# Kernel tuning notes

Measured on AMD Instinct MI355X. Metric: run time of the kernel, lower is better.

Reference implementation:

```python
import jax, jax.numpy as jnp
import numpy as np

# Dimensions inferred from the module (few-shot reweighted YOLOv2 region loss)
B, C, NA, NCPA = 64, 20, 5, 1          # batch, base classes, anchors, classes-per-anchor
H, W = 19, 19                           # feature map (608 input / stride 32)
T = 50                                  # cfg.max_boxes
THRESH = 0.6
COORD_SCALE = 1.0
CLASS_SCALE = 1.0
NB = B * C                              # per-class 'image' rows, as in the torch code
A4 = NA * H * W
EPS = 1e-12
BCE_EPS = 1e-7
ANCHORS = [[1.3221, 1.73145], [3.19275, 4.00944], [5.05587, 8.09892], [9.47112, 4.84053], [11.2364, 10.0071]]


def iou_xywh(x1, y1, w1, h1, x2, y2, w2, h2):
    # center-size IoU, matches darknet bbox_iou(x1y1x2y2=False)
    l = jnp.maximum(x1 - w1 * 0.5, x2 - w2 * 0.5)
    r = jnp.minimum(x1 + w1 * 0.5, x2 + w2 * 0.5)
    t = jnp.maximum(y1 - h1 * 0.5, y2 - h2 * 0.5)
    b = jnp.minimum(y1 + h1 * 0.5, y2 + h2 * 0.5)
    inter = jnp.clip(r - l, 0.0) * jnp.clip(b - t, 0.0)
    union = w1 * h1 + w2 * h2 - inter
    return inter / jnp.maximum(union, EPS)


def setup_inputs() -> dict:
    key = jax.random.key(0)
    k1, k2, k3, k4 = jax.random.split(key, 4)
    output = jax.random.normal(k1, (NB, NA * (5 + NCPA), H, W), jnp.float32) * 0.5
    # target rows: [cls, x, y, w, h] * T, coords in (0,1); x kept > 0 so all boxes are 'valid'
    cls_ids = jax.random.randint(k2, (B, C, T), 0, C).astype(jnp.float32)
    xy = jax.random.uniform(k3, (B, C, T, 2), minval=0.05, maxval=0.95)
    wh = jax.random.uniform(k4, (B, C, T, 2), minval=0.05, maxval=0.5)
    target = jnp.concatenate([cls_ids[..., None], xy, wh], axis=-1).reshape(B, C, T * 5)
    anchors = jnp.asarray(ANCHORS, jnp.float32)
    return {"output": output, "target": target, "anchors": anchors}


def _forward(output, target, anchors):
    target = jax.lax.stop_gradient(target)
    anchors = jax.lax.stop_gradient(anchors)
    out5 = output.reshape(NB, NA, 5 + NCPA, H, W)
    x = jax.nn.sigmoid(out5[:, :, 0])
    y = jax.nn.sigmoid(out5[:, :, 1])
    w = out5[:, :, 2]
    h = out5[:, :, 3]
    conf = jax.nn.sigmoid(out5[:, :, 4])
    # class logits regrouped to original batch: (B*NA*H*W, C)
    cls = out5[:, :, 5:5 + NCPA].reshape(NB, NA, H, W)
    cls_logits = cls.reshape(B, C, NA * H * W).transpose(0, 2, 1).reshape(-1, C)
    # decode pred boxes (detached, mirroring torch's use of .data)
    grid_x = jnp.arange(W, dtype=jnp.float32)[None, None, None, :]
    grid_y = jnp.arange(H, dtype=jnp.float32)[None, None, :, None]
    aw = anchors[:, 0][None, :, None, None]
    ah = anchors[:, 1][None, :, None, None]
    px = jax.lax.stop_gradient(x) + grid_x
    py = jax.lax.stop_gradient(y) + grid_y
    pw = jnp.exp(jax.lax.stop_gradient(w)) * aw
    ph = jnp.exp(jax.lax.stop_gradient(h)) * ah
    # ground-truth boxes per row
    tgt = target.reshape(NB, T, 5)
    cls_t = tgt[:, :, 0]
    gx = tgt[:, :, 1] * W
    gy = tgt[:, :, 2] * H
    gw = tgt[:, :, 3] * W
    gh = tgt[:, :, 4] * H
    # 'break on first zero x' semantics
    valid = jnp.cumprod((tgt[:, :, 1] != 0).astype(jnp.int32), axis=1) > 0
    # stage 1: zero conf_mask where any gt IoU > thresh (scan over T to avoid (NB,T,A4) blowup)
    pxf = px.reshape(NB, A4); pyf = py.reshape(NB, A4)
    pwf = pw.reshape(NB, A4); phf = ph.reshape(NB, A4)

    def iou_step(ci, xs):
        gxt, gyt, gwt, ght, vt = xs
        iou = iou_xywh(pxf, pyf, pwf, phf, gxt[:, None], gyt[:, None], gwt[:, None], ght[:, None])
        return jnp.maximum(ci, jnp.where(vt[:, None], iou, 0.0)), None

    cur_ious, _ = jax.lax.scan(iou_step, jnp.zeros((NB, A4), jnp.float32), (gx.T, gy.T, gw.T, gh.T, valid.T))
    conf_mask0 = jnp.where(cur_ious.reshape(NB, NA, H, W) > THRESH, 0.0, 1.0)
    # best anchor per gt by wh-only IoU
    inter = jnp.minimum(gw[..., None], anchors[:, 0]) * jnp.minimum(gh[..., None], anchors[:, 1])
    union = gw[..., None] * gh[..., None] + anchors[:, 0] * anchors[:, 1] - inter
    best_n = jnp.argmax(inter / jnp.maximum(union, EPS), axis=-1).astype(jnp.int32)  # (NB,T)
    gi = gx.astype(jnp.int32)
    gj = gy.astype(jnp.int32)
    # stage 2: ordered scatter of targets (later boxes overwrite earlier, as in the torch loops)
    binds = jnp.arange(NB)
    z = jnp.zeros((NB, NA, H, W), jnp.float32)
    # seen < 12800 branch: tx=ty=0.5, tw=th=0, coord_mask=1
    carry0 = (jnp.ones_like(z), z, conf_mask0, jnp.full_like(z, 0.5), jnp.full_like(z, 0.5), z, z, z, z)

    def tgt_step(carry, xs):
        cm, clm, cfm, tx, ty, tw, th, tconf, tcls = carry
        gxt, gyt, gwt, ght, bn, git, gjt, vt, ct = xs
        idx = (binds, bn, gjt, git)

        def upd(arr, val):
            return arr.at[idx].set(jnp.where(vt, val, arr[idx]))

        aw_b = anchors[bn, 0]
        ah_b = anchors[bn, 1]
        iou = iou_xywh(gxt, gyt, gwt, ght, px[idx], py[idx], pw[idx], ph[idx])
        cm = upd(cm, 1.0)
        clm = upd(clm, 1.0)
        cfm = upd(cfm, 1.0)
        tx = upd(tx, gxt - git.astype(jnp.float32))
        ty = upd(ty, gyt - gjt.astype(jnp.float32))
        tw = upd(tw, jnp.log(jnp.maximum(gwt, EPS) / aw_b))
        th = upd(th, jnp.log(jnp.maximum(ght, EPS) / ah_b))
        tconf = upd(tconf, iou)
        tcls = upd(tcls, ct)
        return (cm, clm, cfm, tx, ty, tw, th, tconf, tcls), None

    xs = (gx.T, gy.T, gw.T, gh.T, best_n.T, gi.T, gj.T, valid.T, cls_t.T)
    (coord_mask, cls_mask, conf_mask, tx, ty, tw, th, tconf, tcls), _ = jax.lax.scan(tgt_step, carry0, xs)
    # regroup per-class rows back to original batch (neg_ratio='full' -> counts[i] == C)
    cm_grp = cls_mask.reshape(B, C, NA, H, W).sum(axis=1)
    tcls_grp = tcls.reshape(B, C, NA, H, W).sum(axis=1)
    sel = (cm_grp == 1.0).reshape(-1)           # exclude colliding cells
    labels = tcls_grp.reshape(-1).astype(jnp.int32)

    def bce_mean(p, t):
        p = jnp.clip(p, BCE_EPS, 1.0 - BCE_EPS)
        return jnp.mean(-(t * jnp.log(p) + (1.0 - t) * jnp.log(1.0 - p)))

    loss_x = COORD_SCALE * bce_mean(x * coord_mask, tx * coord_mask)
    loss_y = COORD_SCALE * bce_mean(y * coord_mask, ty * coord_mask)
    loss_w = COORD_SCALE * 0.5 * jnp.mean((w * coord_mask - tw * coord_mask) ** 2)
    loss_h = COORD_SCALE * 0.5 * jnp.mean((h * coord_mask - th * coord_mask) ** 2)
    loss_conf = 0.5 * jnp.mean((conf * conf_mask - tconf * conf_mask) ** 2)
    logp = jax.nn.log_softmax(cls_logits, axis=-1)
    nll = -jnp.take_along_axis(logp, labels[:, None], axis=1)[:, 0]
    nsel = jnp.maximum(jnp.sum(sel.astype(jnp.float32)), 1.0)
    loss_cls = CLASS_SCALE * jnp.sum(jnp.where(sel, nll, 0.0)) / nsel
    return loss_x + loss_y + loss_w + loss_h + loss_conf + loss_cls


def reference(output, target, anchors):
    return _forward(output, target, anchors)
```

## Files before the change

kernel.cpp:

```cpp
#include <hip/hip_runtime.h>
#include <math.h>

constexpr int cB   = 64;
constexpr int cC   = 20;
constexpr int cNA  = 5;
constexpr int cH   = 19;
constexpr int cW   = 19;
constexpr int cT   = 50;
constexpr int cNB  = cB * cC;
constexpr int cHW  = cH * cW;
constexpr int cA4  = cNA * cHW;
constexpr int cCH  = cNA * 6;
constexpr long cNTOT = (long)cNB * cA4;
constexpr int cCLS_BLOCKS = cB * cNA;

__device__ __constant__ float cAW[cNA]   = {1.3221f, 3.19275f, 5.05587f, 9.47112f, 11.2364f};
__device__ __constant__ float cAH[cNA]   = {1.73145f, 4.00944f, 8.09892f, 4.84053f, 10.0071f};
__device__ __constant__ float cAREA[cNA] = {2.28930345f, 12.80114796f, 40.94706183f, 45.84455262f, 112.44377644f};
__device__ __constant__ float cLNAW[cNA] = {0.27920469f, 1.16088088f, 1.62060702f, 2.24822684f, 2.41915174f};
__device__ __constant__ float cLNAH[cNA] = {0.54896100f, 1.38865236f, 2.09173157f, 1.57701337f, 2.30329495f};

constexpr int ACC_BANKS = 64;
constexpr size_t OFF_CNT = 2560;
constexpr size_t OFF_ROW = 4096;
constexpr size_t ZERO_BYTES = OFF_ROW + (size_t)cB * cA4 * 4;

__device__ __forceinline__ float fexp(float x) {
    return __builtin_amdgcn_exp2f(x * 1.4426950408889634f);
}
__device__ __forceinline__ float flog(float x) {
    return __builtin_amdgcn_logf(x) * 0.6931471805599453f;
}
__device__ __forceinline__ float frcp(float x) { return __builtin_amdgcn_rcpf(x); }
__device__ __forceinline__ float fsigmoid(float x) { return frcp(1.0f + fexp(-x)); }

typedef _Float16 h2 __attribute__((ext_vector_type(2)));
union HU { unsigned u; h2 h; };
__device__ __forceinline__ unsigned splat2(float v) {
    HU x; _Float16 f = (_Float16)v; x.h[0] = f; x.h[1] = f; return x.u;
}
constexpr float cS = 1.2649110640673518f;

__launch_bounds__(256)
__global__ void k_main(const float* __restrict__ outp, const float* __restrict__ target,
                       int* __restrict__ rowenc, double* __restrict__ acc) {
    __shared__ int s_win[cA4];
    __shared__ int s_tc[cT];
    __shared__ __align__(16) unsigned s_box[cT][8];
    __shared__ __align__(16) float4 s_gt[cT];
    __shared__ double s_red[3][4];
    const int tid  = threadIdx.x;
    const int nb   = blockIdx.x >> 1;
    const int half = blockIdx.x & 1;
    const int base = (half << 10) + tid;
    const int b_   = nb / cC;
    const int c_   = nb - b_ * cC;
    const float* obase = outp + (size_t)nb * (cCH * cHW);

    for (int k = tid; k < cA4; k += 256) s_win[k] = -1;
    __syncthreads();

    if (tid < 64) {
        const int t = tid;
        float xr = 1.f, yr = 0.f, wr = 0.f, hr = 0.f;
        if (t < cT) {
            const float* tg = target + (size_t)nb * (cT * 5) + t * 5;
            xr = tg[1]; yr = tg[2]; wr = tg[3]; hr = tg[4];
        }
        unsigned long long nz = __ballot(xr != 0.0f);
        if (t < cT) {
            unsigned long long below = (2ull << t) - 1ull;
            bool valid = ((~nz) & below) == 0ull;
            float gx = xr * (float)cW, gy = yr * (float)cH;
            float gw = wr * (float)cW, gh = hr * (float)cH;
            s_gt[t] = make_float4(gx, gy, gw, gh);
            if (valid) {
                s_box[t][0] = splat2(cS * (gx - 0.5f * gw));
                s_box[t][1] = splat2(cS * (gx + 0.5f * gw));
                s_box[t][2] = splat2(cS * (gy - 0.5f * gh));
                s_box[t][3] = splat2(cS * (gy + 0.5f * gh));
                s_box[t][4] = splat2(-0.6f * (gw * gh));
                float garea = gw * gh;
                float best = -1.0f; int bn = 0;
                for (int n = 0; n < cNA; ++n) {
                    float inter = fminf(gw, cAW[n]) * fminf(gh, cAH[n]);
                    float uni   = garea + cAREA[n] - inter;
                    float r = inter / fmaxf(uni, 1e-12f);
                    if (r > best) { best = r; bn = n; }
                }
                int cell = bn * cHW + (int)gy * cW + (int)gx;
                s_tc[t] = cell;
                atomicMax(&s_win[cell], t);
            } else {
                s_box[t][0] = splat2(1e4f);  s_box[t][1] = splat2(-1e4f);
                s_box[t][2] = splat2(1e4f);  s_box[t][3] = splat2(-1e4f);
                s_box[t][4] = splat2(0.0f);
                s_tc[t] = -1;
            }
        }
    }
    __syncthreads();
    if (half == 0 && tid < cT) {
        int cell = s_tc[tid];
        if (cell >= 0 && s_win[cell] == tid)
            atomicAdd(&rowenc[b_ * cA4 + cell], (1 << 10) | (c_ * cT + tid));
    }

    h2 pl2[2], pr2[2], pt2[2], pb2[2], ov2[2], pa06h[2];
    float conf[4], tcf[4];
    unsigned wbits = 0;
    float bce = 0.0f, sq = 0.0f;
    const h2 z2 = { (_Float16)0.0f, (_Float16)0.0f };

    #pragma unroll
    for (int u = 0; u < 4; ++u) {
        int cell = base + (u << 8);
        bool a_  = cell < cA4;
        int cc   = a_ ? cell : (cA4 - 1);
        int na   = cc / cHW;
        int rem  = cc - na * cHW;
        int j    = rem / cW;
        int i    = rem - j * cW;
        const float* ob = obase + (size_t)(na * 6) * cHW + rem;
        float xl = ob[0], yl = ob[cHW], wl = ob[2*cHW], hl = ob[3*cHW], cl = ob[4*cHW];
        float aw = cAW[na], ah = cAH[na];
        float x  = fsigmoid(xl), y = fsigmoid(yl), cf = fsigmoid(cl);
        float px = x + (float)i, py = y + (float)j;
        float pw = fexp(wl) * aw, ph = fexp(hl) * ah;
        float l0 = px - 0.5f*pw, r0 = px + 0.5f*pw;
        float t0 = py - 0.5f*ph, b0 = py + 0.5f*ph;
        float pa = pw * ph;
        int p = u >> 1, s = u & 1;
        pl2[p][s] = (_Float16)(cS * l0);  pr2[p][s] = (_Float16)(cS * r0);
        pt2[p][s] = (_Float16)(cS * t0);  pb2[p][s] = (_Float16)(cS * b0);
        pa06h[p][s] = (_Float16)(0.6f * pa);
        ov2[p][s] = (_Float16)0.0f;
        conf[u] = cf; tcf[u] = 0.0f;

        float tx = 0.5f, ty = 0.5f, tw = 0.0f, th = 0.0f;
        int wt = s_win[cc];
        bool wfl = (wt >= 0) && a_;
        if (wfl) {
            wbits |= (1u << u);
            float4 g = s_gt[wt];
            float gx = g.x, gy = g.y, gw = g.z, gh = g.w;
            tx = gx - (float)i; ty = gy - (float)j;
            tw = flog(fmaxf(gw, 1e-12f)) - cLNAW[na];
            th = flog(fmaxf(gh, 1e-12f)) - cLNAH[na];
            float iw = fminf(r0, gx + 0.5f*gw) - fmaxf(l0, gx - 0.5f*gw);
            float ih = fminf(b0, gy + 0.5f*gh) - fmaxf(t0, gy - 0.5f*gh);
            iw = fmaxf(iw, 0.0f); ih = fmaxf(ih, 0.0f);
            float inter = iw * ih;
            float uni   = gw*gh + pa - inter;
            tcf[u] = inter * frcp(fmaxf(uni, 1e-12f));
        }
        if (a_) {
            float pc = fminf(fmaxf(x, 1e-7f), 1.0f - 1e-7f);
            bce += -(tx * flog(pc) + (1.0f - tx) * flog(1.0f - pc));
            pc = fminf(fmaxf(y, 1e-7f), 1.0f - 1e-7f);
            bce += -(ty * flog(pc) + (1.0f - ty) * flog(1.0f - pc));
            float dw = wl - tw, dh = hl - th;
            sq += dw*dw + dh*dh;
        }
    }

    #pragma unroll 10
    for (int t = 0; t < cT; ++t) {
        uint4 bx = *(const uint4*)&s_box[t][0];
        unsigned gv = s_box[t][4];
        HU a, b, c, d, e;
        a.u = bx.x; b.u = bx.y; c.u = bx.z; d.u = bx.w; e.u = gv;
        #pragma unroll
        for (int p = 0; p < 2; ++p) {
            h2 iw = __builtin_elementwise_min(pr2[p], b.h) - __builtin_elementwise_max(pl2[p], a.h);
            h2 ih = __builtin_elementwise_min(pb2[p], d.h) - __builtin_elementwise_max(pt2[p], c.h);
            iw = __builtin_elementwise_max(iw, z2);
            ih = __builtin_elementwise_max(ih, z2);
            ov2[p] = __builtin_elementwise_max(ov2[p], iw * ih + e.h);
        }
    }

    float sc = 0.0f;
    #pragma unroll
    for (int u = 0; u < 4; ++u) {
        int cell = base + (u << 8);
        if (cell >= cA4) continue;
        int p = u >> 1, s = u & 1;
        bool wfl  = (wbits >> u) & 1;
        bool over = ov2[p][s] > pa06h[p][s];
        float cm  = wfl ? 1.0f : (over ? 0.0f : 1.0f);
        float d   = (conf[u] - tcf[u]) * cm;
        sc += d * d;
    }

    double v0 = (double)bce, v1 = (double)sq, v2 = (double)sc;
    for (int off = 32; off > 0; off >>= 1) {
        v0 += __shfl_down(v0, off);
        v1 += __shfl_down(v1, off);
        v2 += __shfl_down(v2, off);
    }
    int lane = tid & 63, wid = tid >> 6;
    if (lane == 0) { s_red[0][wid] = v0; s_red[1][wid] = v1; s_red[2][wid] = v2; }
    __syncthreads();
    if (tid == 0) {
        double a0 = s_red[0][0] + s_red[0][1] + s_red[0][2] + s_red[0][3];
        double a1 = s_red[1][0] + s_red[1][1] + s_red[1][2] + s_red[1][3];
        double a2 = s_red[2][0] + s_red[2][1] + s_red[2][2] + s_red[2][3];
        int bank = blockIdx.x & (ACC_BANKS - 1);
        atomicAdd(&acc[0*ACC_BANKS + bank], a0);
        atomicAdd(&acc[1*ACC_BANKS + bank], a1);
        atomicAdd(&acc[2*ACC_BANKS + bank], a2);
    }
}

__launch_bounds__(384)
__global__ void k_cls(const float* __restrict__ outp, const float* __restrict__ target,
                      const int* __restrict__ rowenc, double* __restrict__ acc,
                      int* __restrict__ cnt, float* __restrict__ out) {
    __shared__ double s_red[2][6];
    __shared__ int s_last;
    const int tid = threadIdx.x;
    const int b   = blockIdx.x / cNA;
    const int na  = blockIdx.x - b * cNA;
    double nll = 0.0, ns = 0.0;
    if (tid < cHW) {
        const int rem = tid;
        const float* ob = outp + ((size_t)(b * cC) * cCH + na * 6 + 5) * cHW + rem;
        float l[cC]; float m = -1e30f;
        #pragma unroll
        for (int c = 0; c < cC; ++c) {
            l[c] = ob[(size_t)c * (cCH * cHW)];
            m = fmaxf(m, l[c]);
        }
        float s = 0.0f;
        #pragma unroll
        for (int c = 0; c < cC; ++c) s += fexp(l[c] - m);
        float lse = m + flog(s);
        int row = b * cA4 + na * cHW + rem;
        int v = rowenc[row];
        if ((v >> 10) == 1) {
            int payload = v & 1023;
            int selc = payload / cT;
            int selt = payload - selc * cT;
            int label = (int)target[((size_t)(b * cC + selc) * cT + selt) * 5];
            nll = (double)(lse - l[label]);
            ns  = 1.0;
        }
    }
    for (int off = 32; off > 0; off >>= 1) {
        nll += __shfl_down(nll, off);
        ns  += __shfl_down(ns, off);
    }
    int lane = tid & 63, wid = tid >> 6;
    if (lane == 0) { s_red[0][wid] = nll; s_red[1][wid] = ns; }
    __syncthreads();
    if (tid == 0) {
        double a0 = 0.0, a1 = 0.0;
        #pragma unroll
        for (int w = 0; w < 6; ++w) { a0 += s_red[0][w]; a1 += s_red[1][w]; }
        int bank = blockIdx.x & (ACC_BANKS - 1);
        atomicAdd(&acc[3*ACC_BANKS + bank], a0);
        atomicAdd(&acc[4*ACC_BANKS + bank], a1);
        __threadfence();
        s_last = (atomicAdd(cnt, 1) == cCLS_BLOCKS - 1);
    }
    __syncthreads();
    if (s_last && tid < 64) {
        __threadfence();
        double s[5];
        #pragma unroll
        for (int j = 0; j < 5; ++j) {
            double v = atomicAdd(&acc[j * ACC_BANKS + tid], 0.0);
            for (int off = 32; off > 0; off >>= 1) v += __shfl_down(v, off);
            s[j] = v;
        }
        if (tid == 0) {
            double Ninv = 1.0 / (double)cNTOT;
            double loss = s[0] * Ninv
                        + 0.5 * s[1] * Ninv
                        + 0.5 * s[2] * Ninv
                        + s[3] / fmax(s[4], 1.0);
            out[0] = (float)loss;
        }
    }
}

extern "C" void kernel_launch(void* const* d_in, const int* in_sizes, int n_in,
                              void* d_out, int out_size, void* d_ws, size_t ws_size,
                              hipStream_t stream) {
    const float* output = (const float*)d_in[0];
    const float* target = (const float*)d_in[1];
    char* ws = (char*)d_ws;
    double* acc    = (double*)ws;
    int*    cnt    = (int*)(ws + OFF_CNT);
    int*    rowenc = (int*)(ws + OFF_ROW);

    hipMemsetAsync(ws, 0, ZERO_BYTES, stream);

    k_main<<<cNB * 2, 256, 0, stream>>>(output, target, rowenc, acc);
    k_cls<<<cCLS_BLOCKS, 384, 0, stream>>>(output, target, rowenc, acc, cnt, (float*)d_out);
}
```

Measured before the change: 128.9 us.

## Drop memset and atomics; recompute class winners in cls kernel, use per-block partials

Removes the hipMemsetAsync launch and the global atomic rowenc table. The class kernel now recomputes per-class target winners for its (batch, anchor) slice in shared memory, and both kernels write per-block partial sums that the last block reduces. The cnt reset moves into k_main. The class-logit loads and softmax now run only for selected cells. This removes one launch and the atomic contention, at the cost of redundant target parsing in k_cls.

Result: slower. 134.4 us (+4.3%).

```diff
diff --git a/kernel.cpp b/kernel.cpp
--- a/kernel.cpp
+++ b/kernel.cpp
@@ -12,7 +12,8 @@
 constexpr int cA4  = cNA * cHW;
 constexpr int cCH  = cNA * 6;
 constexpr long cNTOT = (long)cNB * cA4;
-constexpr int cCLS_BLOCKS = cB * cNA;
+constexpr int cMAIN_BLOCKS = cNB * 2;
+constexpr int cCLS_BLOCKS  = cB * cNA;
 
 __device__ __constant__ float cAW[cNA]   = {1.3221f, 3.19275f, 5.05587f, 9.47112f, 11.2364f};
 __device__ __constant__ float cAH[cNA]   = {1.73145f, 4.00944f, 8.09892f, 4.84053f, 10.0071f};
@@ -20,10 +21,9 @@
 __device__ __constant__ float cLNAW[cNA] = {0.27920469f, 1.16088088f, 1.62060702f, 2.24822684f, 2.41915174f};
 __device__ __constant__ float cLNAH[cNA] = {0.54896100f, 1.38865236f, 2.09173157f, 1.57701337f, 2.30329495f};
 
-constexpr int ACC_BANKS = 64;
-constexpr size_t OFF_CNT = 2560;
-constexpr size_t OFF_ROW = 4096;
-constexpr size_t ZERO_BYTES = OFF_ROW + (size_t)cB * cA4 * 4;
+constexpr size_t OFF_P1  = 0;
+constexpr size_t OFF_CNT = (size_t)cMAIN_BLOCKS * 3 * 8;
+constexpr size_t OFF_P2  = OFF_CNT + 64;
 
 __device__ __forceinline__ float fexp(float x) {
     return __builtin_amdgcn_exp2f(x * 1.4426950408889634f);
@@ -43,9 +43,8 @@
 
 __launch_bounds__(256)
 __global__ void k_main(const float* __restrict__ outp, const float* __restrict__ target,
-                       int* __restrict__ rowenc, double* __restrict__ acc) {
+                       double* __restrict__ part1, int* __restrict__ cnt) {
     __shared__ int s_win[cA4];
-    __shared__ int s_tc[cT];
     __shared__ __align__(16) unsigned s_box[cT][8];
     __shared__ __align__(16) float4 s_gt[cT];
     __shared__ double s_red[3][4];
@@ -53,9 +52,9 @@
     const int nb   = blockIdx.x >> 1;
     const int half = blockIdx.x & 1;
     const int base = (half << 10) + tid;
-    const int b_   = nb / cC;
-    const int c_   = nb - b_ * cC;
     const float* obase = outp + (size_t)nb * (cCH * cHW);
+
+    if (blockIdx.x == 0 && tid == 0) *cnt = 0;
 
     for (int k = tid; k < cA4; k += 256) s_win[k] = -1;
     __syncthreads();
@@ -89,22 +88,15 @@
                     if (r > best) { best = r; bn = n; }
                 }
                 int cell = bn * cHW + (int)gy * cW + (int)gx;
-                s_tc[t] = cell;
                 atomicMax(&s_win[cell], t);
             } else {
                 s_box[t][0] = splat2(1e4f);  s_box[t][1] = splat2(-1e4f);
                 s_box[t][2] = splat2(1e4f);  s_box[t][3] = splat2(-1e4f);
                 s_box[t][4] = splat2(0.0f);
-                s_tc[t] = -1;
             }
         }
     }
     __syncthreads();
-    if (half == 0 && tid < cT) {
-        int cell = s_tc[tid];
-        if (cell >= 0 && s_win[cell] == tid)
-            atomicAdd(&rowenc[b_ * cA4 + cell], (1 << 10) | (c_ * cT + tid));
-    }
 
     h2 pl2[2], pr2[2], pt2[2], pb2[2], ov2[2], pa06h[2];
     float conf[4], tcf[4];
@@ -203,45 +195,76 @@
     if (lane == 0) { s_red[0][wid] = v0; s_red[1][wid] = v1; s_red[2][wid] = v2; }
     __syncthreads();
     if (tid == 0) {
-        double a0 = s_red[0][0] + s_red[0][1] + s_red[0][2] + s_red[0][3];
-        double a1 = s_red[1][0] + s_red[1][1] + s_red[1][2] + s_red[1][3];
-        double a2 = s_red[2][0] + s_red[2][1] + s_red[2][2] + s_red[2][3];
-        int bank = blockIdx.x & (ACC_BANKS - 1);
-        atomicAdd(&acc[0*ACC_BANKS + bank], a0);
-        atomicAdd(&acc[1*ACC_BANKS + bank], a1);
-        atomicAdd(&acc[2*ACC_BANKS + bank], a2);
+        part1[(size_t)blockIdx.x * 3 + 0] = s_red[0][0] + s_red[0][1] + s_red[0][2] + s_red[0][3];
+        part1[(size_t)blockIdx.x * 3 + 1] = s_red[1][0] + s_red[1][1] + s_red[1][2] + s_red[1][3];
+        part1[(size_t)blockIdx.x * 3 + 2] = s_red[2][0] + s_red[2][1] + s_red[2][2] + s_red[2][3];
     }
 }
 
 __launch_bounds__(384)
 __global__ void k_cls(const float* __restrict__ outp, const float* __restrict__ target,
-                      const int* __restrict__ rowenc, double* __restrict__ acc,
+                      const double* __restrict__ part1, double* __restrict__ part2,
                       int* __restrict__ cnt, float* __restrict__ out) {
+    __shared__ int s_win[cC * cHW];
     __shared__ double s_red[2][6];
+    __shared__ double s_fin[5][6];
     __shared__ int s_last;
-    const int tid = threadIdx.x;
-    const int b   = blockIdx.x / cNA;
-    const int na  = blockIdx.x - b * cNA;
+    const int tid  = threadIdx.x;
+    const int wave = tid >> 6;
+    const int lane = tid & 63;
+    const int b    = blockIdx.x / cNA;
+    const int na   = blockIdx.x - b * cNA;
+
+    for (int k = tid; k < cC * cHW; k += 384) s_win[k] = -1;
+    __syncthreads();
+
+    for (int c = wave; c < cC; c += 6) {
+        const float* tg = target + (size_t)(b * cC + c) * (cT * 5);
+        float xr = 1.f, yr = 0.f, wr = 0.f, hr = 0.f;
+        if (lane < cT) { xr = tg[lane*5+1]; yr = tg[lane*5+2]; wr = tg[lane*5+3]; hr = tg[lane*5+4]; }
+        unsigned long long nz = __ballot(xr != 0.0f);
+        if (lane < cT) {
+            unsigned long long below = (2ull << lane) - 1ull;
+            bool valid = ((~nz) & below) == 0ull;
+            if (valid) {
+                float gx = xr * (float)cW, gy = yr * (float)cH;
+                float gw = wr * (float)cW, gh = hr * (float)cH;
+                float garea = gw * gh;
+                float best = -1.0f; int bn = 0;
+                for (int n = 0; n < cNA; ++n) {
+                    float inter = fminf(gw, cAW[n]) * fminf(gh, cAH[n]);
+                    float uni   = garea + cAREA[n] - inter;
+                    float r = inter / fmaxf(uni, 1e-12f);
+                    if (r > best) { best = r; bn = n; }
+                }
+                if (bn == na)
+                    atomicMax(&s_win[c * cHW + (int)gy * cW + (int)gx], lane);
+            }
+        }
+    }
+    __syncthreads();
+
     double nll = 0.0, ns = 0.0;
     if (tid < cHW) {
         const int rem = tid;
-        const float* ob = outp + ((size_t)(b * cC) * cCH + na * 6 + 5) * cHW + rem;
-        float l[cC]; float m = -1e30f;
+        int cntc = 0, selc = -1, selt = -1;
         #pragma unroll
         for (int c = 0; c < cC; ++c) {
-            l[c] = ob[(size_t)c * (cCH * cHW)];
-            m = fmaxf(m, l[c]);
-        }
-        float s = 0.0f;
-        #pragma unroll
-        for (int c = 0; c < cC; ++c) s += fexp(l[c] - m);
-        float lse = m + flog(s);
-        int row = b * cA4 + na * cHW + rem;
-        int v = rowenc[row];
-        if ((v >> 10) == 1) {
-            int payload = v & 1023;
-            int selc = payload / cT;
-            int selt = payload - selc * cT;
+            int wv = s_win[c * cHW + rem];
+            if (wv >= 0) { cntc++; selc = c; selt = wv; }
+        }
+        if (cntc == 1) {
+            const float* ob = outp + ((size_t)(b * cC) * cCH + na * 6 + 5) * cHW + rem;
+            float l[cC]; float m = -1e30f;
+            #pragma unroll
+            for (int c = 0; c < cC; ++c) {
+                l[c] = ob[(size_t)c * (cCH * cHW)];
+                m = fmaxf(m, l[c]);
+            }
+            float s = 0.0f;
+            #pragma unroll
+            for (int c = 0; c < cC; ++c) s += fexp(l[c] - m);
+            float lse = m + flog(s);
             int label = (int)target[((size_t)(b * cC + selc) * cT + selt) * 5];
             nll = (double)(lse - l[label]);
             ns  = 1.0;
@@ -251,30 +274,48 @@
         nll += __shfl_down(nll, off);
         ns  += __shfl_down(ns, off);
     }
-    int lane = tid & 63, wid = tid >> 6;
-    if (lane == 0) { s_red[0][wid] = nll; s_red[1][wid] = ns; }
+    if (lane == 0) { s_red[0][wave] = nll; s_red[1][wave] = ns; }
     __syncthreads();
     if (tid == 0) {
         double a0 = 0.0, a1 = 0.0;
         #pragma unroll
         for (int w = 0; w < 6; ++w) { a0 += s_red[0][w]; a1 += s_red[1][w]; }
-        int bank = blockIdx.x & (ACC_BANKS - 1);
-        atomicAdd(&acc[3*ACC_BANKS + bank], a0);
-        atomicAdd(&acc[4*ACC_BANKS + bank], a1);
+        part2[(size_t)blockIdx.x * 2 + 0] = a0;
+        part2[(size_t)blockIdx.x * 2 + 1] = a1;
         __threadfence();
         s_last = (atomicAdd(cnt, 1) == cCLS_BLOCKS - 1);
     }
     __syncthreads();
-    if (s_last && tid < 64) {
+
+    if (s_last) {
         __threadfence();
-        double s[5];
+        double v[5] = {0.0, 0.0, 0.0, 0.0, 0.0};
+        for (int k = tid; k < cMAIN_BLOCKS; k += 384) {
+            v[0] += part1[(size_t)k * 3 + 0];
+            v[1] += part1[(size_t)k * 3 + 1];
+            v[2] += part1[(size_t)k * 3 + 2];
+        }
+        for (int k = tid; k < cCLS_BLOCKS; k += 384) {
+            v[3] += atomicAdd(&part2[(size_t)k * 2 + 0], 0.0);
+            v[4] += atomicAdd(&part2[(size_t)k * 2 + 1], 0.0);
+        }
         #pragma unroll
-        for (int j = 0; j < 5; ++j) {
-            double v = atomicAdd(&acc[j * ACC_BANKS + tid], 0.0);
-            for (int off = 32; off > 0; off >>= 1) v += __shfl_down(v, off);
-            s[j] = v;
-        }
+        for (int j = 0; j < 5; ++j)
+            for (int off = 32; off > 0; off >>= 1) v[j] += __shfl_down(v[j], off);
+        if (lane == 0) {
+            #pragma unroll
+            for (int j = 0; j < 5; ++j) s_fin[j][wave] = v[j];
+        }
+        __syncthreads();
         if (tid == 0) {
+            double s[5];
+            #pragma unroll
+            for (int j = 0; j < 5; ++j) {
+                double a = 0.0;
+                #pragma unroll
+                for (int w = 0; w < 6; ++w) a += s_fin[j][w];
+                s[j] = a;
+            }
             double Ninv = 1.0 / (double)cNTOT;
             double loss = s[0] * Ninv
                         + 0.5 * s[1] * Ninv
@@ -291,12 +332,10 @@
     const float* output = (const float*)d_in[0];
     const float* target = (const float*)d_in[1];
     char* ws = (char*)d_ws;
-    double* acc    = (double*)ws;
-    int*    cnt    = (int*)(ws + OFF_CNT);
-    int*    rowenc = (int*)(ws + OFF_ROW);
-
-    hipMemsetAsync(ws, 0, ZERO_BYTES, stream);
-
-    k_main<<<cNB * 2, 256, 0, stream>>>(output, target, rowenc, acc);
-    k_cls<<<cCLS_BLOCKS, 384, 0, stream>>>(output, target, rowenc, acc, cnt, (float*)d_out);
-}
+    double* part1 = (double*)(ws + OFF_P1);
+    int*    cnt   = (int*)   (ws + OFF_CNT);
+    double* part2 = (double*)(ws + OFF_P2);
+
+    k_main<<<cMAIN_BLOCKS, 256, 0, stream>>>(output, target, part1, cnt);
+    k_cls<<<cCLS_BLOCKS, 384, 0, stream>>>(output, target, part1, part2, cnt, (float*)d_out);
+}
```

## Merge k_main half-blocks into one 512-thread block; split k_cls blocks in two

Applied to the files above, without the earlier changes.

k_main now runs one 512-thread block per class-image row instead of two 256-thread halves. The target preprocessing, IoU setup and shared-memory init that each half repeated now run once per row. k_cls is split into twice as many 192-thread blocks, each covering half the grid cells of an anchor, so the gather-heavy class loss uses more, smaller blocks. The trade-off is fewer, larger main blocks, which puts more register pressure on each CU and may lower its occupancy.

New measurement: 133.8 us. +3.8%, slower.

```diff
diff --git a/kernel.cpp b/kernel.cpp
--- a/kernel.cpp
+++ b/kernel.cpp
@@ -12,7 +12,7 @@
 constexpr int cA4  = cNA * cHW;
 constexpr int cCH  = cNA * 6;
 constexpr long cNTOT = (long)cNB * cA4;
-constexpr int cCLS_BLOCKS = cB * cNA;
+constexpr int cCLS_BLOCKS = cB * cNA * 2;
 
 __device__ __constant__ float cAW[cNA]   = {1.3221f, 3.19275f, 5.05587f, 9.47112f, 11.2364f};
 __device__ __constant__ float cAH[cNA]   = {1.73145f, 4.00944f, 8.09892f, 4.84053f, 10.0071f};
@@ -41,23 +41,21 @@
 }
 constexpr float cS = 1.2649110640673518f;
 
-__launch_bounds__(256)
+__launch_bounds__(512, 8)
 __global__ void k_main(const float* __restrict__ outp, const float* __restrict__ target,
                        int* __restrict__ rowenc, double* __restrict__ acc) {
     __shared__ int s_win[cA4];
     __shared__ int s_tc[cT];
     __shared__ __align__(16) unsigned s_box[cT][8];
     __shared__ __align__(16) float4 s_gt[cT];
-    __shared__ double s_red[3][4];
-    const int tid  = threadIdx.x;
-    const int nb   = blockIdx.x >> 1;
-    const int half = blockIdx.x & 1;
-    const int base = (half << 10) + tid;
-    const int b_   = nb / cC;
-    const int c_   = nb - b_ * cC;
+    __shared__ double s_red[3][8];
+    const int tid = threadIdx.x;
+    const int nb  = blockIdx.x;
+    const int b_  = nb / cC;
+    const int c_  = nb - b_ * cC;
     const float* obase = outp + (size_t)nb * (cCH * cHW);
 
-    for (int k = tid; k < cA4; k += 256) s_win[k] = -1;
+    for (int k = tid; k < cA4; k += 512) s_win[k] = -1;
     __syncthreads();
 
     if (tid < 64) {
@@ -100,7 +98,7 @@
         }
     }
     __syncthreads();
-    if (half == 0 && tid < cT) {
+    if (tid < cT) {
         int cell = s_tc[tid];
         if (cell >= 0 && s_win[cell] == tid)
             atomicAdd(&rowenc[b_ * cA4 + cell], (1 << 10) | (c_ * cT + tid));
@@ -114,7 +112,7 @@
 
     #pragma unroll
     for (int u = 0; u < 4; ++u) {
-        int cell = base + (u << 8);
+        int cell = tid + (u << 9);
         bool a_  = cell < cA4;
         int cc   = a_ ? cell : (cA4 - 1);
         int na   = cc / cHW;
@@ -183,7 +181,7 @@
     float sc = 0.0f;
     #pragma unroll
     for (int u = 0; u < 4; ++u) {
-        int cell = base + (u << 8);
+        int cell = tid + (u << 9);
         if (cell >= cA4) continue;
         int p = u >> 1, s = u & 1;
         bool wfl  = (wbits >> u) & 1;
@@ -203,28 +201,31 @@
     if (lane == 0) { s_red[0][wid] = v0; s_red[1][wid] = v1; s_red[2][wid] = v2; }
     __syncthreads();
     if (tid == 0) {
-        double a0 = s_red[0][0] + s_red[0][1] + s_red[0][2] + s_red[0][3];
-        double a1 = s_red[1][0] + s_red[1][1] + s_red[1][2] + s_red[1][3];
-        double a2 = s_red[2][0] + s_red[2][1] + s_red[2][2] + s_red[2][3];
-        int bank = blockIdx.x & (ACC_BANKS - 1);
+        double a0 = 0.0, a1 = 0.0, a2 = 0.0;
+        #pragma unroll
+        for (int w = 0; w < 8; ++w) { a0 += s_red[0][w]; a1 += s_red[1][w]; a2 += s_red[2][w]; }
+        int bank = nb & (ACC_BANKS - 1);
         atomicAdd(&acc[0*ACC_BANKS + bank], a0);
         atomicAdd(&acc[1*ACC_BANKS + bank], a1);
         atomicAdd(&acc[2*ACC_BANKS + bank], a2);
     }
 }
 
-__launch_bounds__(384)
+__launch_bounds__(192)
 __global__ void k_cls(const float* __restrict__ outp, const float* __restrict__ target,
                       const int* __restrict__ rowenc, double* __restrict__ acc,
                       int* __restrict__ cnt, float* __restrict__ out) {
-    __shared__ double s_red[2][6];
+    __shared__ double s_red[2][3];
     __shared__ int s_last;
-    const int tid = threadIdx.x;
-    const int b   = blockIdx.x / cNA;
-    const int na  = blockIdx.x - b * cNA;
+    const int tid  = threadIdx.x;
+    const int blk  = blockIdx.x;
+    const int b    = blk / (cNA * 2);
+    const int r2   = blk - b * (cNA * 2);
+    const int na   = r2 >> 1;
+    const int half = r2 & 1;
+    const int rem  = half * 192 + tid;
     double nll = 0.0, ns = 0.0;
-    if (tid < cHW) {
-        const int rem = tid;
+    if (rem < cHW) {
         const float* ob = outp + ((size_t)(b * cC) * cCH + na * 6 + 5) * cHW + rem;
         float l[cC]; float m = -1e30f;
         #pragma unroll
@@ -236,8 +237,7 @@
         #pragma unroll
         for (int c = 0; c < cC; ++c) s += fexp(l[c] - m);
         float lse = m + flog(s);
-        int row = b * cA4 + na * cHW + rem;
-        int v = rowenc[row];
+        int v = rowenc[b * cA4 + na * cHW + rem];
         if ((v >> 10) == 1) {
             int payload = v & 1023;
             int selc = payload / cT;
@@ -255,10 +255,9 @@
     if (lane == 0) { s_red[0][wid] = nll; s_red[1][wid] = ns; }
     __syncthreads();
     if (tid == 0) {
-        double a0 = 0.0, a1 = 0.0;
-        #pragma unroll
-        for (int w = 0; w < 6; ++w) { a0 += s_red[0][w]; a1 += s_red[1][w]; }
-        int bank = blockIdx.x & (ACC_BANKS - 1);
+        double a0 = s_red[0][0] + s_red[0][1] + s_red[0][2];
+        double a1 = s_red[1][0] + s_red[1][1] + s_red[1][2];
+        int bank = blk & (ACC_BANKS - 1);
         atomicAdd(&acc[3*ACC_BANKS + bank], a0);
         atomicAdd(&acc[4*ACC_BANKS + bank], a1);
         __threadfence();
@@ -297,6 +296,6 @@
 
     hipMemsetAsync(ws, 0, ZERO_BYTES, stream);
 
-    k_main<<<cNB * 2, 256, 0, stream>>>(output, target, rowenc, acc);
-    k_cls<<<cCLS_BLOCKS, 384, 0, stream>>>(output, target, rowenc, acc, cnt, (float*)d_out);
-}
+    k_main<<<cNB, 512, 0, stream>>>(output, target, rowenc, acc);
+    k_cls<<<cCLS_BLOCKS, 192, 0, stream>>>(output, target, rowenc, acc, cnt, (float*)d_out);
+}
```
